# Kernel tuning notes

Hardware: AMD Instinct MI355X
Metric: run time of the kernel (lower is better)

Reference implementation:

```python
import jax, jax.numpy as jnp
import numpy as np

ITER_N = 3  # iterNum
DIM = 256   # channel dim entering MPNCOV
# static flat indices of the upper triangle (row-major of dim*dim), as in Triuvec
_TRIU_I, _TRIU_J = np.triu_indices(DIM)
TRIU_IDX = jnp.asarray(_TRIU_I * DIM + _TRIU_J)


def setup_inputs() -> dict:
    key = jax.random.key(0)
    x = jax.random.normal(key, (256, 256, 14, 14), dtype=jnp.float32)
    return {"x": x}


def reference(x):
    B, C, H, W = x.shape
    M = H * W
    xr = x.reshape(B, C, M)
    # Covpool: y = x @ I_hat @ x^T with I_hat = (1/M)(I - (1/M) 1 1^T)
    # equivalently (1/M) * centered Gram matrix
    xc = xr - xr.mean(axis=2, keepdims=True)
    cov = jnp.einsum('bcm,bdm->bcd', xc, xc) / M  # [B, C, C]
    # Sqrtm: Newton-Schulz iteration (iSQRT-COV)
    I = jnp.eye(C, dtype=x.dtype)
    normA = jnp.trace(cov, axis1=1, axis2=2)  # = (1/3)*sum(cov * 3I)
    A = cov / normA[:, None, None]
    ZY = 0.5 * (3.0 * I - A)
    Yk = jnp.matmul(A, ZY)
    Zk = ZY
    for _ in range(ITER_N - 2):
        ZY = 0.5 * (3.0 * I - jnp.matmul(Zk, Yk))
        Yk = jnp.matmul(Yk, ZY)
        Zk = jnp.matmul(ZY, Zk)
    YZY = 0.5 * jnp.matmul(Yk, 3.0 * I - jnp.matmul(Zk, Yk))
    y = YZY * jnp.sqrt(normA)[:, None, None]
    # Triuvec: extract upper-triangular entries, [B, C*(C+1)/2]
    return y.reshape(B, C * C)[:, TRIU_IDX]
```

## Files before the change

kernel.cpp:

```cpp
#include <hip/hip_runtime.h>
#include <math.h>

#define BB 256
#define CC 256
#define MN 196
#define TRI 32896

#define MSC 32.0f
#define INV_MSC  (1.0f/32.0f)
#define INV_MSC2 (1.0f/1024.0f)

typedef _Float16 f16;
typedef f16   f16x8 __attribute__((ext_vector_type(8)));
typedef float f32x4 __attribute__((ext_vector_type(4)));
typedef unsigned u32x4 __attribute__((ext_vector_type(4)));

__device__ __forceinline__ unsigned pack_split(float v) {
    f16 h = (f16)v;
    f16 l = (f16)(v - (float)h);
    return (unsigned)__builtin_bit_cast(unsigned short, h) |
           ((unsigned)__builtin_bit_cast(unsigned short, l) << 16);
}
__device__ __forceinline__ float unpack_split(unsigned w) {
    f16 h = __builtin_bit_cast(f16, (unsigned short)(w & 0xffffu));
    f16 l = __builtin_bit_cast(f16, (unsigned short)(w >> 16));
    return (float)h + (float)l;
}
__device__ __forceinline__ f16x8 swap_pairs(f16x8 v) {
    return __builtin_shufflevector(v, v, 1, 0, 3, 2, 5, 4, 7, 6);
}
__device__ __forceinline__ void gload_lds16(const unsigned* g, const f16* l) {
    __builtin_amdgcn_global_load_lds(
        (__attribute__((address_space(1))) void*)(size_t)g,
        (__attribute__((address_space(3))) void*)(unsigned)(size_t)l,
        16, 0, 0);
}

__global__ __launch_bounds__(256) void meanvar_kernel(const float* __restrict__ x,
                                                      float* __restrict__ mu,
                                                      float* __restrict__ vr) {
    int wave = (blockIdx.x * 256 + threadIdx.x) >> 6;
    int lane = threadIdx.x & 63;
    const float* row = x + (size_t)wave * MN;
    float a0 = row[lane], a1 = row[lane + 64], a2 = row[lane + 128];
    float a3 = (lane < MN - 192) ? row[lane + 192] : 0.0f;
    float s = a0 + a1 + a2 + a3;
    float q = a0 * a0 + a1 * a1 + a2 * a2 + a3 * a3;
    #pragma unroll
    for (int off = 32; off > 0; off >>= 1) {
        s += __shfl_down(s, off, 64);
        q += __shfl_down(q, off, 64);
    }
    if (lane == 0) {
        float m = s * (1.0f / MN);
        mu[wave] = m;
        vr[wave] = q * (1.0f / MN) - m * m;
    }
}

__global__ __launch_bounds__(256) void norm_kernel(const float* __restrict__ vr,
                                                   float* __restrict__ inv,
                                                   float* __restrict__ snorm,
                                                   float* __restrict__ invs) {
    __shared__ float red[256];
    int b = blockIdx.x, i = threadIdx.x;
    red[i] = vr[b * CC + i];
    __syncthreads();
    for (int s = 128; s > 0; s >>= 1) {
        if (i < s) red[i] += red[i + s];
        __syncthreads();
    }
    if (i == 0) {
        float n = red[0];
        inv[b] = 1.0f / n;
        float sq = sqrtf(n);
        snorm[b] = sq;
        invs[b] = 1.0f / sq;
    }
}

__global__ __launch_bounds__(256) void xsplit_kernel(const float* __restrict__ x,
                                                     const float* __restrict__ mu,
                                                     unsigned* __restrict__ xs, int b0) {
    int wave = (blockIdx.x * 256 + threadIdx.x) >> 6;
    int lane = threadIdx.x & 63;
    int bl = wave >> 8;
    int c  = wave & 255;
    int bg = b0 + bl;
    const float* row = x + ((size_t)bg * CC + c) * MN;
    float m = mu[bg * CC + c];
    unsigned* orow = xs + (size_t)bl * (CC * 208) + (size_t)c * 208;
    orow[lane]       = pack_split(MSC * (row[lane] - m));
    orow[lane + 64]  = pack_split(MSC * (row[lane + 64] - m));
    orow[lane + 128] = pack_split(MSC * (row[lane + 128] - m));
    if (lane < 4)       orow[lane + 192] = pack_split(MSC * (row[lane + 192] - m));
    else if (lane < 16) orow[lane + 192] = 0u;
}

template <int MODE>
__global__ __launch_bounds__(512) void gemm512(const unsigned* __restrict__ Ag,
                                               const unsigned* __restrict__ Bg,
                                               const unsigned* __restrict__ Eg,
                                               void* __restrict__ Cg,
                                               const float alpha0, const float beta0,
                                               const float diag_add,
                                               const float* __restrict__ Sg, int b0) {
    constexpr int    LDK = (MODE == 2) ? 208 : 256;
    constexpr int    KCH = (MODE == 2) ? 13  : 16;
    constexpr size_t BST = (MODE == 2) ? (size_t)CC * 208 : (size_t)CC * CC;
    __shared__ __align__(16) f16 As[2][4096];
    __shared__ __align__(16) f16 Bs[2][4096];
    const int bl = blockIdx.x / 3;
    const int t  = blockIdx.x - 3 * bl;
    const int bg = b0 + bl;
    const int ti = (t == 2) ? 1 : 0;
    const int tj = (t == 0) ? 0 : 1;
    const int tid  = threadIdx.x;
    const int lane = tid & 63;
    const int wid  = tid >> 6;
    const int wrow = wid >> 2, wcol = wid & 3;

    const unsigned* Abase = Ag + (size_t)bl * BST + (size_t)(ti * 128) * LDK;
    const unsigned* Bbase = Bg + (size_t)bl * BST + (size_t)(tj * 128) * LDK;

    const int sw = wid & 3;
    const unsigned* gsrc = (wid < 4) ? Abase : Bbase;
    const int srow0 = sw * 32 + (lane >> 2);
    const int sslot = (lane & 3) ^ ((lane >> 3) & 3);
    const unsigned* gsl = gsrc + (size_t)srow0 * LDK + sslot * 4;
    f16* lbase = ((wid < 4) ? &As[0][0] : &Bs[0][0]) + sw * 1024;

    int aoff[4], boff[2];
    #pragma unroll
    for (int ib = 0; ib < 4; ++ib) {
        int ra = wrow * 64 + ib * 16 + (lane & 15);
        aoff[ib] = ra * 64 + ((((lane >> 4) ^ (ra >> 1)) & 3) << 4);
    }
    #pragma unroll
    for (int jb = 0; jb < 2; ++jb) {
        int rb = wcol * 32 + jb * 16 + (lane & 15);
        boff[jb] = rb * 64 + ((((lane >> 4) ^ (rb >> 1)) & 3) << 4);
    }

    f32x4 acc[4][2];
    #pragma unroll
    for (int i = 0; i < 4; ++i)
        #pragma unroll
        for (int j = 0; j < 2; ++j) acc[i][j] = 0.0f;

    auto STAGE = [&](int nb, int ks) {
        const unsigned* s = gsl + ks * 16;
        f16* d = lbase + nb * 4096;
        gload_lds16(s, d);
        gload_lds16(s + (size_t)16 * LDK, d + 512);
    };

    STAGE(0, 0);
    __syncthreads();
    #pragma unroll 2
    for (int ks = 0; ks < KCH; ++ks) {
        const int nb = ks & 1;
        if (ks + 1 < KCH) STAGE(nb ^ 1, ks + 1);
        const char* Ab8 = (const char*)As + nb * 8192;
        const char* Bb8 = (const char*)Bs + nb * 8192;
        f16x8 av[4], bv[2], bw[2];
        #pragma unroll
        for (int ib = 0; ib < 4; ++ib)
            av[ib] = *(const f16x8*)(Ab8 + aoff[ib]);
        #pragma unroll
        for (int jb = 0; jb < 2; ++jb) {
            bv[jb] = *(const f16x8*)(Bb8 + boff[jb]);
            bw[jb] = swap_pairs(bv[jb]);
        }
        #pragma unroll
        for (int ib = 0; ib < 4; ++ib)
            #pragma unroll
            for (int jb = 0; jb < 2; ++jb) {
                acc[ib][jb] = __builtin_amdgcn_mfma_f32_16x16x32_f16(av[ib], bv[jb], acc[ib][jb], 0, 0, 0);
                acc[ib][jb] = __builtin_amdgcn_mfma_f32_16x16x32_f16(av[ib], bw[jb], acc[ib][jb], 0, 0, 0);
            }
        __syncthreads();
    }

    const int gi0base = ti * 128 + wrow * 64 + ((lane >> 4) << 2);
    const int gjbase  = tj * 128 + wcol * 32 + (lane & 15);

    if (MODE != 1) {
        float sc = (Sg != nullptr) ? Sg[bg] : 1.0f;
        float al = alpha0 * sc;
        float be = beta0 * sc;
        unsigned* Cb = (unsigned*)Cg + (size_t)bl * CC * CC;
        const unsigned* Eb = (Eg != nullptr) ? Eg + (size_t)bl * CC * CC : nullptr;
        #pragma unroll
        for (int ib = 0; ib < 4; ++ib) {
            #pragma unroll
            for (int jb = 0; jb < 2; ++jb) {
                int gi0 = gi0base + ib * 16;
                int gj  = gjbase + jb * 16;
                unsigned pk[4];
                #pragma unroll
                for (int q = 0; q < 4; ++q) {
                    int gi = gi0 + q;
                    float val = al * acc[ib][jb][q];
                    if (Eb) val += be * unpack_split(Eb[(size_t)gi * CC + gj]);
                    if (gi == gj) val += diag_add;
                    unsigned w = pack_split(val);
                    pk[q] = w;
                    Cb[(size_t)gi * CC + gj] = w;
                }
                if (ti != tj) {
                    u32x4 m = {pk[0], pk[1], pk[2], pk[3]};
                    *(u32x4*)&Cb[(size_t)gj * CC + gi0] = m;
                }
            }
        }
    } else {
        float* ob = (float*)Cg + (size_t)bg * TRI;
        #pragma unroll
        for (int ib = 0; ib < 4; ++ib) {
            #pragma unroll
            for (int jb = 0; jb < 2; ++jb) {
                int gi0 = gi0base + ib * 16;
                int gj  = gjbase + jb * 16;
                #pragma unroll
                for (int q = 0; q < 4; ++q) {
                    int gi = gi0 + q;
                    if (gj >= gi)
                        ((float*)Cg + (size_t)bg * TRI)[gi * CC - (gi * (gi - 1)) / 2 - gi + gj]
                            = acc[ib][jb][q] * INV_MSC2;
                }
                (void)ob;
            }
        }
    }
}

extern "C" void kernel_launch(void* const* d_in, const int* in_sizes, int n_in,
                              void* d_out, int out_size, void* d_ws, size_t ws_size,
                              hipStream_t stream) {
    const float* x = (const float*)d_in[0];
    float* out = (float*)d_out;
    unsigned* ws = (unsigned*)d_ws;

    const int SCR = 2 * BB * CC + 3 * BB;
    float* mu    = out + (out_size - SCR);
    float* vr    = mu + BB * CC;
    float* inv   = vr + BB * CC;
    float* snorm = inv + BB;
    float* invs  = snorm + BB;

    size_t per_b = 4ull * CC * CC * sizeof(unsigned);
    int gmax = (int)(ws_size / per_b);
    int g = 1;
    while (g * 2 <= gmax && g * 2 <= BB) g *= 2;

    size_t slotf = (size_t)g * CC * CC;
    unsigned* s0 = ws;
    unsigned* s1 = ws + slotf;
    unsigned* s2 = ws + 2 * slotf;
    unsigned* s3 = ws + 3 * slotf;

    meanvar_kernel<<<BB * CC / 4, 256, 0, stream>>>(x, mu, vr);
    norm_kernel<<<BB, 256, 0, stream>>>(vr, inv, snorm, invs);

    for (int b0 = 0; b0 < BB; b0 += g) {
        xsplit_kernel<<<g * 64, 256, 0, stream>>>(x, mu, s1, b0);
        gemm512<2><<<g * 3, 512, 0, stream>>>(s1, s1, nullptr, (void*)s0,
                                              1.0f / (MSC * MN), 0.0f, 0.0f, inv, b0);
        gemm512<0><<<g * 3, 512, 0, stream>>>(s0, s0, s0, (void*)s1, -0.5f * INV_MSC, 1.5f, 0.0f, nullptr, b0);
        gemm512<0><<<g * 3, 512, 0, stream>>>(s0, s1, s1, (void*)s2, 0.25f * INV_MSC, -0.75f, 1.5f * MSC, nullptr, b0);
        gemm512<0><<<g * 3, 512, 0, stream>>>(s1, s2, nullptr, (void*)s3, INV_MSC, 0.0f, 0.0f, snorm, b0);
        gemm512<0><<<g * 3, 512, 0, stream>>>(s2, s0, s2, (void*)s1, -0.5f * INV_MSC, 1.5f, 0.0f, invs, b0);
        gemm512<0><<<g * 3, 512, 0, stream>>>(s1, s3, nullptr, (void*)s0, -0.5f * INV_MSC, 0.0f, 1.5f * MSC, nullptr, b0);
        gemm512<1><<<g * 3, 512, 0, stream>>>(s3, s0, nullptr, d_out, 0.0f, 0.0f, 0.0f, nullptr, b0);
    }
}
```

Measured before the change: 419.2 us.

## Fuse mean/variance into split kernel, widen GEMM K-chunk, stage epilogue through LDS

Mean and variance are now computed inside xsplit_kernel from values already in registers, so the separate meanvar pass and one read of x go away. The norm kernel now runs per batch group. The GEMM's K-chunk per stage grows from 16 to 32 (64KB of LDS, 8-way XOR swizzle, padded K of 224), which halves the number of barriers. The epilogue stages the E tile and the output tile through LDS for coalesced 16-byte global reads and writes. The cost is lower occupancy from the larger LDS footprint and extra barriers in the epilogue.

```diff
diff --git a/kernel.cpp b/kernel.cpp
--- a/kernel.cpp
+++ b/kernel.cpp
@@ -36,51 +36,8 @@
         16, 0, 0);
 }
 
-__global__ __launch_bounds__(256) void meanvar_kernel(const float* __restrict__ x,
-                                                      float* __restrict__ mu,
-                                                      float* __restrict__ vr) {
-    int wave = (blockIdx.x * 256 + threadIdx.x) >> 6;
-    int lane = threadIdx.x & 63;
-    const float* row = x + (size_t)wave * MN;
-    float a0 = row[lane], a1 = row[lane + 64], a2 = row[lane + 128];
-    float a3 = (lane < MN - 192) ? row[lane + 192] : 0.0f;
-    float s = a0 + a1 + a2 + a3;
-    float q = a0 * a0 + a1 * a1 + a2 * a2 + a3 * a3;
-    #pragma unroll
-    for (int off = 32; off > 0; off >>= 1) {
-        s += __shfl_down(s, off, 64);
-        q += __shfl_down(q, off, 64);
-    }
-    if (lane == 0) {
-        float m = s * (1.0f / MN);
-        mu[wave] = m;
-        vr[wave] = q * (1.0f / MN) - m * m;
-    }
-}
-
-__global__ __launch_bounds__(256) void norm_kernel(const float* __restrict__ vr,
-                                                   float* __restrict__ inv,
-                                                   float* __restrict__ snorm,
-                                                   float* __restrict__ invs) {
-    __shared__ float red[256];
-    int b = blockIdx.x, i = threadIdx.x;
-    red[i] = vr[b * CC + i];
-    __syncthreads();
-    for (int s = 128; s > 0; s >>= 1) {
-        if (i < s) red[i] += red[i + s];
-        __syncthreads();
-    }
-    if (i == 0) {
-        float n = red[0];
-        inv[b] = 1.0f / n;
-        float sq = sqrtf(n);
-        snorm[b] = sq;
-        invs[b] = 1.0f / sq;
-    }
-}
-
 __global__ __launch_bounds__(256) void xsplit_kernel(const float* __restrict__ x,
-                                                     const float* __restrict__ mu,
+                                                     float* __restrict__ vr,
                                                      unsigned* __restrict__ xs, int b0) {
     int wave = (blockIdx.x * 256 + threadIdx.x) >> 6;
     int lane = threadIdx.x & 63;
@@ -88,13 +45,44 @@
     int c  = wave & 255;
     int bg = b0 + bl;
     const float* row = x + ((size_t)bg * CC + c) * MN;
-    float m = mu[bg * CC + c];
-    unsigned* orow = xs + (size_t)bl * (CC * 208) + (size_t)c * 208;
-    orow[lane]       = pack_split(MSC * (row[lane] - m));
-    orow[lane + 64]  = pack_split(MSC * (row[lane + 64] - m));
-    orow[lane + 128] = pack_split(MSC * (row[lane + 128] - m));
-    if (lane < 4)       orow[lane + 192] = pack_split(MSC * (row[lane + 192] - m));
-    else if (lane < 16) orow[lane + 192] = 0u;
+    float a0 = row[lane], a1 = row[lane + 64], a2 = row[lane + 128];
+    float a3 = (lane < MN - 192) ? row[lane + 192] : 0.0f;
+    float s = a0 + a1 + a2 + a3;
+    float q = a0 * a0 + a1 * a1 + a2 * a2 + a3 * a3;
+    #pragma unroll
+    for (int off = 32; off > 0; off >>= 1) {
+        s += __shfl_xor(s, off, 64);
+        q += __shfl_xor(q, off, 64);
+    }
+    float m = s * (1.0f / MN);
+    if (lane == 0) vr[bg * CC + c] = q * (1.0f / MN) - m * m;
+    unsigned* orow = xs + (size_t)bl * (CC * 224) + (size_t)c * 224;
+    orow[lane]       = pack_split(MSC * (a0 - m));
+    orow[lane + 64]  = pack_split(MSC * (a1 - m));
+    orow[lane + 128] = pack_split(MSC * (a2 - m));
+    if (lane < 4)       orow[lane + 192] = pack_split(MSC * (a3 - m));
+    else if (lane < 32) orow[lane + 192] = 0u;
+}
+
+__global__ __launch_bounds__(256) void norm_kernel(const float* __restrict__ vr,
+                                                   float* __restrict__ inv,
+                                                   float* __restrict__ snorm,
+                                                   float* __restrict__ invs, int b0) {
+    __shared__ float red[256];
+    int b = b0 + blockIdx.x, i = threadIdx.x;
+    red[i] = vr[b * CC + i];
+    __syncthreads();
+    for (int s = 128; s > 0; s >>= 1) {
+        if (i < s) red[i] += red[i + s];
+        __syncthreads();
+    }
+    if (i == 0) {
+        float n = red[0];
+        inv[b] = 1.0f / n;
+        float sq = sqrtf(n);
+        snorm[b] = sq;
+        invs[b] = 1.0f / sq;
+    }
 }
 
 template <int MODE>
@@ -105,11 +93,14 @@
                                                const float alpha0, const float beta0,
                                                const float diag_add,
                                                const float* __restrict__ Sg, int b0) {
-    constexpr int    LDK = (MODE == 2) ? 208 : 256;
-    constexpr int    KCH = (MODE == 2) ? 13  : 16;
-    constexpr size_t BST = (MODE == 2) ? (size_t)CC * 208 : (size_t)CC * CC;
-    __shared__ __align__(16) f16 As[2][4096];
-    __shared__ __align__(16) f16 Bs[2][4096];
+    constexpr int    LDK = (MODE == 2) ? 224 : 256;
+    constexpr int    KCH = LDK / 32;
+    constexpr size_t BST = (size_t)CC * LDK;
+    __shared__ __align__(16) unsigned char smem[65536];
+    f16* AsBuf = (f16*)smem;
+    f16* BsBuf = (f16*)(smem + 32768);
+    unsigned* tile = (unsigned*)smem;
+
     const int bl = blockIdx.x / 3;
     const int t  = blockIdx.x - 3 * bl;
     const int bg = b0 + bl;
@@ -125,21 +116,24 @@
 
     const int sw = wid & 3;
     const unsigned* gsrc = (wid < 4) ? Abase : Bbase;
-    const int srow0 = sw * 32 + (lane >> 2);
-    const int sslot = (lane & 3) ^ ((lane >> 3) & 3);
-    const unsigned* gsl = gsrc + (size_t)srow0 * LDK + sslot * 4;
-    f16* lbase = ((wid < 4) ? &As[0][0] : &Bs[0][0]) + sw * 1024;
-
-    int aoff[4], boff[2];
+    const unsigned* gsl = gsrc + (size_t)(sw * 32 + (lane >> 3)) * LDK
+                               + (((lane & 7) ^ ((lane >> 3) & 7)) << 2);
+    f16* mbase = (wid < 4) ? AsBuf : BsBuf;
+
+    int aoff[4][2], boff[2][2];
     #pragma unroll
     for (int ib = 0; ib < 4; ++ib) {
-        int ra = wrow * 64 + ib * 16 + (lane & 15);
-        aoff[ib] = ra * 64 + ((((lane >> 4) ^ (ra >> 1)) & 3) << 4);
+        int r = wrow * 64 + ib * 16 + (lane & 15);
+        #pragma unroll
+        for (int tt = 0; tt < 2; ++tt)
+            aoff[ib][tt] = r * 128 + ((((tt * 4) + (lane >> 4)) ^ (r & 7)) << 4);
     }
     #pragma unroll
     for (int jb = 0; jb < 2; ++jb) {
-        int rb = wcol * 32 + jb * 16 + (lane & 15);
-        boff[jb] = rb * 64 + ((((lane >> 4) ^ (rb >> 1)) & 3) << 4);
+        int r = wcol * 32 + jb * 16 + (lane & 15);
+        #pragma unroll
+        for (int tt = 0; tt < 2; ++tt)
+            boff[jb][tt] = r * 128 + ((((tt * 4) + (lane >> 4)) ^ (r & 7)) << 4);
     }
 
     f32x4 acc[4][2];
@@ -149,41 +143,47 @@
         for (int j = 0; j < 2; ++j) acc[i][j] = 0.0f;
 
     auto STAGE = [&](int nb, int ks) {
-        const unsigned* s = gsl + ks * 16;
-        f16* d = lbase + nb * 4096;
-        gload_lds16(s, d);
-        gload_lds16(s + (size_t)16 * LDK, d + 512);
+        const unsigned* s = gsl + (size_t)ks * 32;
+        f16* d = mbase + nb * 8192 + sw * 2048;
+        #pragma unroll
+        for (int i = 0; i < 4; ++i)
+            gload_lds16(s + (size_t)i * 8 * LDK, d + i * 512);
     };
 
     STAGE(0, 0);
     __syncthreads();
-    #pragma unroll 2
+    #pragma unroll 1
     for (int ks = 0; ks < KCH; ++ks) {
         const int nb = ks & 1;
         if (ks + 1 < KCH) STAGE(nb ^ 1, ks + 1);
-        const char* Ab8 = (const char*)As + nb * 8192;
-        const char* Bb8 = (const char*)Bs + nb * 8192;
-        f16x8 av[4], bv[2], bw[2];
-        #pragma unroll
-        for (int ib = 0; ib < 4; ++ib)
-            av[ib] = *(const f16x8*)(Ab8 + aoff[ib]);
-        #pragma unroll
-        for (int jb = 0; jb < 2; ++jb) {
-            bv[jb] = *(const f16x8*)(Bb8 + boff[jb]);
-            bw[jb] = swap_pairs(bv[jb]);
+        const char* Ab8 = (const char*)(AsBuf + nb * 8192);
+        const char* Bb8 = (const char*)(BsBuf + nb * 8192);
+        #pragma unroll
+        for (int tt = 0; tt < 2; ++tt) {
+            f16x8 av[4], bv[2], bw[2];
+            #pragma unroll
+            for (int ib = 0; ib < 4; ++ib)
+                av[ib] = *(const f16x8*)(Ab8 + aoff[ib][tt]);
+            #pragma unroll
+            for (int jb = 0; jb < 2; ++jb) {
+                bv[jb] = *(const f16x8*)(Bb8 + boff[jb][tt]);
+                bw[jb] = swap_pairs(bv[jb]);
+            }
+            #pragma unroll
+            for (int ib = 0; ib < 4; ++ib)
+                #pragma unroll
+                for (int jb = 0; jb < 2; ++jb) {
+                    acc[ib][jb] = __builtin_amdgcn_mfma_f32_16x16x32_f16(av[ib], bv[jb], acc[ib][jb], 0, 0, 0);
+                    acc[ib][jb] = __builtin_amdgcn_mfma_f32_16x16x32_f16(av[ib], bw[jb], acc[ib][jb], 0, 0, 0);
+                }
         }
-        #pragma unroll
-        for (int ib = 0; ib < 4; ++ib)
-            #pragma unroll
-            for (int jb = 0; jb < 2; ++jb) {
-                acc[ib][jb] = __builtin_amdgcn_mfma_f32_16x16x32_f16(av[ib], bv[jb], acc[ib][jb], 0, 0, 0);
-                acc[ib][jb] = __builtin_amdgcn_mfma_f32_16x16x32_f16(av[ib], bw[jb], acc[ib][jb], 0, 0, 0);
-            }
         __syncthreads();
     }
 
-    const int gi0base = ti * 128 + wrow * 64 + ((lane >> 4) << 2);
-    const int gjbase  = tj * 128 + wcol * 32 + (lane & 15);
+    const int li0 = wrow * 64 + ((lane >> 4) << 2);
+    const int lj  = wcol * 32 + (lane & 15);
+    const int gi0base = ti * 128 + li0;
+    const int gjbase  = tj * 128 + lj;
 
     if (MODE != 1) {
         float sc = (Sg != nullptr) ? Sg[bg] : 1.0f;
@@ -191,47 +191,76 @@
         float be = beta0 * sc;
         unsigned* Cb = (unsigned*)Cg + (size_t)bl * CC * CC;
         const unsigned* Eb = (Eg != nullptr) ? Eg + (size_t)bl * CC * CC : nullptr;
-        #pragma unroll
-        for (int ib = 0; ib < 4; ++ib) {
+
+        if (Eb) {
+            #pragma unroll
+            for (int it = 0; it < 8; ++it) {
+                int g = it * 512 + tid;
+                int r = g >> 5, c4 = g & 31;
+                *(u32x4*)&tile[r * 128 + c4 * 4] =
+                    *(const u32x4*)&Eb[(size_t)(ti * 128 + r) * CC + tj * 128 + c4 * 4];
+            }
+            __syncthreads();
+        }
+
+        unsigned pk[4][2][4];
+        #pragma unroll
+        for (int ib = 0; ib < 4; ++ib)
+            #pragma unroll
+            for (int jb = 0; jb < 2; ++jb)
+                #pragma unroll
+                for (int q = 0; q < 4; ++q) {
+                    int lr = li0 + q + 16 * ib;
+                    int lc = lj + 16 * jb;
+                    float val = al * acc[ib][jb][q];
+                    if (Eb) val += be * unpack_split(tile[lr * 128 + lc]);
+                    if (gi0base + q + 16 * ib == gjbase + 16 * jb) val += diag_add;
+                    pk[ib][jb][q] = pack_split(val);
+                }
+        __syncthreads();
+
+        #pragma unroll
+        for (int ib = 0; ib < 4; ++ib)
+            #pragma unroll
+            for (int jb = 0; jb < 2; ++jb)
+                #pragma unroll
+                for (int q = 0; q < 4; ++q)
+                    tile[(li0 + q + 16 * ib) * 128 + lj + 16 * jb] = pk[ib][jb][q];
+        __syncthreads();
+
+        #pragma unroll
+        for (int it = 0; it < 8; ++it) {
+            int g = it * 512 + tid;
+            int r = g >> 5, c4 = g & 31;
+            *(u32x4*)&Cb[(size_t)(ti * 128 + r) * CC + tj * 128 + c4 * 4] =
+                *(const u32x4*)&tile[r * 128 + c4 * 4];
+        }
+        if (ti != tj) {
+            #pragma unroll
+            for (int ib = 0; ib < 4; ++ib)
+                #pragma unroll
+                for (int jb = 0; jb < 2; ++jb) {
+                    int gj  = gjbase + 16 * jb;
+                    int gi0 = gi0base + 16 * ib;
+                    u32x4 m = {pk[ib][jb][0], pk[ib][jb][1], pk[ib][jb][2], pk[ib][jb][3]};
+                    *(u32x4*)&Cb[(size_t)gj * CC + gi0] = m;
+                }
+        }
+    } else {
+        float* ob = (float*)Cg + (size_t)bg * TRI;
+        #pragma unroll
+        for (int ib = 0; ib < 4; ++ib)
             #pragma unroll
             for (int jb = 0; jb < 2; ++jb) {
                 int gi0 = gi0base + ib * 16;
                 int gj  = gjbase + jb * 16;
-                unsigned pk[4];
-                #pragma unroll
-                for (int q = 0; q < 4; ++q) {
-                    int gi = gi0 + q;
-                    float val = al * acc[ib][jb][q];
-                    if (Eb) val += be * unpack_split(Eb[(size_t)gi * CC + gj]);
-                    if (gi == gj) val += diag_add;
-                    unsigned w = pack_split(val);
-                    pk[q] = w;
-                    Cb[(size_t)gi * CC + gj] = w;
-                }
-                if (ti != tj) {
-                    u32x4 m = {pk[0], pk[1], pk[2], pk[3]};
-                    *(u32x4*)&Cb[(size_t)gj * CC + gi0] = m;
-                }
-            }
-        }
-    } else {
-        float* ob = (float*)Cg + (size_t)bg * TRI;
-        #pragma unroll
-        for (int ib = 0; ib < 4; ++ib) {
-            #pragma unroll
-            for (int jb = 0; jb < 2; ++jb) {
-                int gi0 = gi0base + ib * 16;
-                int gj  = gjbase + jb * 16;
                 #pragma unroll
                 for (int q = 0; q < 4; ++q) {
                     int gi = gi0 + q;
                     if (gj >= gi)
-                        ((float*)Cg + (size_t)bg * TRI)[gi * CC - (gi * (gi - 1)) / 2 - gi + gj]
-                            = acc[ib][jb][q] * INV_MSC2;
+                        ob[gi * CC - (gi * (gi - 1)) / 2 - gi + gj] = acc[ib][jb][q] * INV_MSC2;
                 }
-                (void)ob;
             }
-        }
     }
 }
 
@@ -242,9 +271,8 @@
     float* out = (float*)d_out;
     unsigned* ws = (unsigned*)d_ws;
 
-    const int SCR = 2 * BB * CC + 3 * BB;
-    float* mu    = out + (out_size - SCR);
-    float* vr    = mu + BB * CC;
+    const int SCR = BB * CC + 3 * BB;
+    float* vr    = out + (out_size - SCR);
     float* inv   = vr + BB * CC;
     float* snorm = inv + BB;
     float* invs  = snorm + BB;
@@ -260,11 +288,9 @@
     unsigned* s2 = ws + 2 * slotf;
     unsigned* s3 = ws + 3 * slotf;
 
-    meanvar_kernel<<<BB * CC / 4, 256, 0, stream>>>(x, mu, vr);
-    norm_kernel<<<BB, 256, 0, stream>>>(vr, inv, snorm, invs);
-
     for (int b0 = 0; b0 < BB; b0 += g) {
-        xsplit_kernel<<<g * 64, 256, 0, stream>>>(x, mu, s1, b0);
+        xsplit_kernel<<<g * 64, 256, 0, stream>>>(x, vr, s1, b0);
+        norm_kernel<<<g, 256, 0, stream>>>(vr, inv, snorm, invs, b0);
         gemm512<2><<<g * 3, 512, 0, stream>>>(s1, s1, nullptr, (void*)s0,
                                               1.0f / (MSC * MN), 0.0f, 0.0f, inv, b0);
         gemm512<0><<<g * 3, 512, 0, stream>>>(s0, s0, s0, (void*)s1, -0.5f * INV_MSC, 1.5f, 0.0f, nullptr, b0);
```

Result: slower. 433.6 us (+3.4%).
